# Kernel optimization log

Measured on AMD Instinct MI355X. Metric: run time of the kernel, lower is better.

Reference implementation:

```python
import jax, jax.numpy as jnp
import numpy as np

EMBED_DIM = 1024
NUM_HEADS = 16
HEAD_DIM = EMBED_DIM // NUM_HEADS


def setup_inputs() -> dict:
    key = jax.random.key(0)
    ks = jax.random.split(key, 7)
    B, S, E = 2, 2048, EMBED_DIM
    # xavier_uniform bound for square [E, E] weight
    bound = float(np.sqrt(6.0 / (E + E)))
    mkw = lambda k: jax.random.uniform(k, (E, E), jnp.float32, -bound, bound)
    return {
        "query": jax.random.normal(ks[0], (B, S, E), jnp.float32),
        "key": jax.random.normal(ks[1], (B, S, E), jnp.float32),
        "value": jax.random.normal(ks[2], (B, S, E), jnp.float32),
        "Wq": mkw(ks[3]),
        "Wk": mkw(ks[4]),
        "Wv": mkw(ks[5]),
        "Wo": mkw(ks[6]),
    }


def reference(query, key, value, Wq, Wk, Wv, Wo):
    # Chunked sigmoid attention: since sigmoid has no cross-key normalization
    # and all projections are bias-free linear maps, summing per-KV-chunk
    # partial outputs is mathematically identical to the full computation:
    #   out = (sigmoid(scale * Q K^T) @ V) @ Wo^T
    B, L, E = query.shape
    H, D = NUM_HEADS, HEAD_DIM
    scale = D ** -0.5
    q = (query @ Wq.T).reshape(B, L, H, D) * scale   # [B,L,H,D]
    k = (key @ Wk.T).reshape(B, -1, H, D)            # [B,S,H,D]
    v = (value @ Wv.T).reshape(B, -1, H, D)          # [B,S,H,D]
    scores = jax.nn.sigmoid(jnp.einsum('blhd,bshd->bhls', q, k))  # [B,H,L,S]
    o = jnp.einsum('bhls,bshd->blhd', scores, v).reshape(B, L, E)
    return o @ Wo.T
```

## Files before the change

kernel.cpp:

```cpp
#include <hip/hip_runtime.h>

typedef float f32x4 __attribute__((ext_vector_type(4)));
typedef float f32x16 __attribute__((ext_vector_type(16)));
typedef __bf16 bf16x4 __attribute__((ext_vector_type(4)));
typedef __bf16 bf16x8 __attribute__((ext_vector_type(8)));

constexpr int E = 1024;
constexpr int S = 2048;
constexpr int Bsz = 2;
constexpr int H = 16;
constexpr int Dh = 64;
constexpr int M = Bsz * S;
constexpr int E2 = 2048;

#define GLOAD_LDS16(g, l)                                                                 \
  __builtin_amdgcn_global_load_lds((const __attribute__((address_space(1))) void*)(g),    \
                                   (__attribute__((address_space(3))) void*)(l), 16, 0, 0)

__device__ __forceinline__ unsigned pk2(float a, float b) {
  union { __bf16 h[2]; unsigned u; } r;
  r.h[0] = (__bf16)a; r.h[1] = (__bf16)b;
  return r.u;
}

__global__ __launch_bounds__(256) void convert_bf16(
    const float* __restrict__ q, const float* __restrict__ k,
    const float* __restrict__ v, const float* __restrict__ wq,
    const float* __restrict__ wk, const float* __restrict__ wv,
    const float* __restrict__ wo, __bf16* __restrict__ aq,
    __bf16* __restrict__ ak, __bf16* __restrict__ av,
    __bf16* __restrict__ wqkv, __bf16* __restrict__ wob) {
  const int id = blockIdx.y;
  const float* src;
  __bf16* dst;
  int n;
  float scale = 1.0f;
  switch (id) {
    case 0: src = q;  dst = aq;             n = M * E; break;
    case 1: src = k;  dst = ak;             n = M * E; break;
    case 2: src = v;  dst = av;             n = M * E; break;
    case 3: src = wq; dst = wqkv;           n = E * E; scale = -0.18033688f; break;
    case 4: src = wk; dst = wqkv + E * E;   n = E * E; break;
    case 5: src = wv; dst = wqkv + 2 * E * E; n = E * E; break;
    default: src = wo; dst = wob;           n = E * E; break;
  }
  const int stride = gridDim.x * 256 * 8;
  for (int i = (blockIdx.x * 256 + threadIdx.x) * 8; i < n; i += stride) {
    f32x4 a = *reinterpret_cast<const f32x4*>(&src[i]);
    f32x4 b = *reinterpret_cast<const f32x4*>(&src[i + 4]);
    bf16x8 o;
    o[0] = (__bf16)(a[0] * scale); o[1] = (__bf16)(a[1] * scale);
    o[2] = (__bf16)(a[2] * scale); o[3] = (__bf16)(a[3] * scale);
    o[4] = (__bf16)(b[0] * scale); o[5] = (__bf16)(b[1] * scale);
    o[6] = (__bf16)(b[2] * scale); o[7] = (__bf16)(b[3] * scale);
    *reinterpret_cast<bf16x8*>(&dst[i]) = o;
  }
}

template <int TM, int MODE, int KS>
__global__ __launch_bounds__(256) void gemm_bf16nt(
    const __bf16* __restrict__ A0, const __bf16* __restrict__ A1,
    const __bf16* __restrict__ A2, const __bf16* __restrict__ Bw,
    void* __restrict__ C0, void* __restrict__ C1, void* __restrict__ C2) {
  static_assert(TM == 64, "vmcnt literal assumes TM=64 (6 chunks/wave)");
  constexpr int MI  = TM / 32;
  constexpr int NT  = KS / 64;
  constexpr int ACH = TM / 8;
  constexpr int NCH = ACH + 16;
  constexpr int NTN = (MODE == 0) ? 24 : 8;
  constexpr int NWG = NTN * (M / TM);
  constexpr int CPX = NWG / 8;

  __shared__ char smem[2][NCH * 1024];

  const int t    = threadIdx.x;
  const int lane = t & 63;
  const int wid  = t >> 6;
  const int wr   = (wid >> 1) * (TM / 2);
  const int wc   = (wid & 1) * 64;
  const int r16  = lane & 15;

  const int bid = blockIdx.x;
  const int fid = (bid & 7) * CPX + (bid >> 3);
  const int mt  = fid / NTN;
  const int nt  = fid % NTN;
  const int tm  = mt * TM;
  const int tn  = nt * 128;
  const int which = tn >> 10;

  const __bf16* Ab = (MODE == 0) ? (which == 0 ? A0 : which == 1 ? A1 : A2) : A0;

  auto stage = [&](int kt, int buf) {
    const int k0  = kt * 64;
    const int k0b = k0 & 1023;
    char* dst = smem[buf];
#pragma unroll
    for (int c = wid; c < NCH; c += 4) {
      const bool isA = c < ACH;
      const int cc   = isA ? c : c - ACH;
      const int L    = cc * 1024 + lane * 16;
      const int row  = L >> 7;
      const int sw   = ((L >> 4) & 7) ^ (row & 7);
      const __bf16* src = isA ? &Ab[(size_t)(tm + row) * KS + k0 + sw * 8]
                              : &Bw[(size_t)(tn + row) * 1024 + k0b + sw * 8];
      GLOAD_LDS16(src, dst + c * 1024);
    }
  };

  stage(0, 0);
  stage(1, 1);

  f32x4 acc[MI][4] = {};

  for (int kt = 0; kt < NT; ++kt) {
    const int buf = kt & 1;
    if (kt + 1 < NT) {
      asm volatile("s_waitcnt vmcnt(6)" ::: "memory");
    } else {
      asm volatile("s_waitcnt vmcnt(0)" ::: "memory");
    }
    __builtin_amdgcn_s_barrier();
    __builtin_amdgcn_sched_barrier(0);

    const __bf16* As = (const __bf16*)smem[buf];
    const __bf16* Bs = (const __bf16*)(smem[buf] + ACH * 1024);

#pragma unroll
    for (int kc = 0; kc < 2; ++kc) {
      bf16x8 af[MI], bfv[4];
#pragma unroll
      for (int mi = 0; mi < MI; ++mi) {
        int row = wr + mi * 16 + r16;
        int g   = (kc * 4 + (lane >> 4)) ^ (row & 7);
        af[mi] = *reinterpret_cast<const bf16x8*>(&As[row * 64 + g * 8]);
      }
#pragma unroll
      for (int ni = 0; ni < 4; ++ni) {
        int row = wc + ni * 16 + r16;
        int g   = (kc * 4 + (lane >> 4)) ^ (row & 7);
        bfv[ni] = *reinterpret_cast<const bf16x8*>(&Bs[row * 64 + g * 8]);
      }
      __builtin_amdgcn_s_setprio(1);
#pragma unroll
      for (int mi = 0; mi < MI; ++mi)
#pragma unroll
        for (int ni = 0; ni < 4; ++ni)
          acc[mi][ni] = __builtin_amdgcn_mfma_f32_16x16x32_bf16(af[mi], bfv[ni],
                                                                acc[mi][ni], 0, 0, 0);
      __builtin_amdgcn_s_setprio(0);
    }

    __builtin_amdgcn_sched_barrier(0);
    __builtin_amdgcn_s_barrier();
    if (kt + 2 < NT) stage(kt + 2, buf);
  }

#pragma unroll
  for (int mi = 0; mi < MI; ++mi) {
#pragma unroll
    for (int ni = 0; ni < 4; ++ni) {
#pragma unroll
      for (int j = 0; j < 4; ++j) {
        float v = acc[mi][ni][j];
        int m = tm + wr + mi * 16 + ((lane >> 4) << 2) + j;
        int n = tn + wc + ni * 16 + r16;
        if constexpr (MODE == 0) {
          int nl = n & 1023;
          int b = m >> 11, s = m & 2047, h = nl >> 6, d = nl & 63;
          __bf16* Cout = which == 0 ? (__bf16*)C0 : which == 1 ? (__bf16*)C1
                                                              : (__bf16*)C2;
          if (which < 2) {
            Cout[((size_t)(b * H + h) * S + s) * Dh + d] = (__bf16)v;
          } else {
            int ssw = (s & ~12) | ((s & 4) << 1) | ((s & 8) >> 1);
            Cout[((size_t)(b * H + h) * Dh + d) * S + ssw] = (__bf16)v;
          }
        } else {
          ((float*)C0)[(size_t)m * E + n] = v;
        }
      }
    }
  }
}

__global__ __launch_bounds__(128, 4) void attn_sigmoid(const __bf16* __restrict__ Q,
                                                       const __bf16* __restrict__ K,
                                                       const __bf16* __restrict__ Vt,
                                                       __bf16* __restrict__ O) {
  __shared__ char smem[16384];

  const int t    = threadIdx.x;
  const int lane = t & 63;
  const int qgrp = t >> 6;
  const int l31  = lane & 31;
  const int hh   = lane >> 5;
  const int qt   = blockIdx.x >> 1;
  const int ss   = blockIdx.x & 1;
  const int q0   = qt * 64;
  const int h    = blockIdx.y;
  const int b    = blockIdx.z;

  const __bf16* Qh = Q + (size_t)(b * H + h) * S * Dh;
  const __bf16* Kh = K + (size_t)(b * H + h) * S * Dh;
  const __bf16* Vh = Vt + (size_t)(b * H + h) * Dh * S;

  const __bf16* kSrc = Kh + (size_t)(ss * 1024 + (lane >> 3)) * Dh +
                       (((lane & 7) ^ (lane >> 3)) * 8);
  const __bf16* vSrc = Vh + (size_t)(lane >> 2) * S + ss * 1024 +
                       (((lane & 3) ^ ((lane >> 3) & 3)) * 8);

  auto stage = [&](int it, int buf) {
    char* dst = smem + buf * 8192;
    if (qgrp == 0) {
#pragma unroll
      for (int j = 0; j < 4; ++j)
        GLOAD_LDS16(kSrc + it * 2048 + j * 512, dst + j * 1024);
    } else {
#pragma unroll
      for (int j = 0; j < 4; ++j)
        GLOAD_LDS16(vSrc + it * 32 + (size_t)j * 16 * S, dst + 4096 + j * 1024);
    }
  };

  bf16x8 Qf[4];
#pragma unroll
  for (int kc = 0; kc < 4; ++kc)
    Qf[kc] = *reinterpret_cast<const bf16x8*>(
        &Qh[(size_t)(q0 + qgrp * 32 + l31) * Dh + kc * 16 + hh * 8]);

  stage(0, 0);
  stage(1, 1);

  f32x16 ot0 = {}, ot1 = {};

#pragma unroll 2
  for (int it = 0; it < 32; ++it) {
    const int buf = it & 1;
    if (it + 1 < 32) {
      asm volatile("s_waitcnt vmcnt(4)" ::: "memory");
    } else {
      asm volatile("s_waitcnt vmcnt(0)" ::: "memory");
    }
    __builtin_amdgcn_s_barrier();
    __builtin_amdgcn_sched_barrier(0);

    const __bf16* Kb = (const __bf16*)(smem + buf * 8192);
    const __bf16* Vb = (const __bf16*)(smem + buf * 8192 + 4096);

    bf16x8 kf[4], vf[4];
#pragma unroll
    for (int kc = 0; kc < 4; ++kc) {
      int x = (2 * kc + hh) ^ (l31 & 7);
      kf[kc] = *reinterpret_cast<const bf16x8*>(&Kb[l31 * 64 + x * 8]);
    }
#pragma unroll
    for (int kc2 = 0; kc2 < 2; ++kc2)
#pragma unroll
      for (int dblk = 0; dblk < 2; ++dblk) {
        int row = dblk * 32 + l31;
        int x   = (2 * kc2 + hh) ^ ((l31 >> 1) & 3);
        vf[kc2 * 2 + dblk] = *reinterpret_cast<const bf16x8*>(&Vb[row * 32 + x * 8]);
      }

    f32x16 sacc = {};
    __builtin_amdgcn_s_setprio(1);
#pragma unroll
    for (int kc = 0; kc < 4; ++kc)
      sacc = __builtin_amdgcn_mfma_f32_32x32x16_bf16(kf[kc], Qf[kc], sacc, 0, 0, 0);
    __builtin_amdgcn_s_setprio(0);

    bf16x8 F[2];
    {
      union { unsigned u[4]; bf16x8 v; } fu[2];
#pragma unroll
      for (int kc2 = 0; kc2 < 2; ++kc2) {
#pragma unroll
        for (int jj = 0; jj < 4; ++jj) {
          float ya = sacc[kc2 * 8 + 2 * jj];
          float yb = sacc[kc2 * 8 + 2 * jj + 1];
          float pa = __builtin_amdgcn_rcpf(1.0f + __builtin_amdgcn_exp2f(ya));
          float pb = __builtin_amdgcn_rcpf(1.0f + __builtin_amdgcn_exp2f(yb));
          fu[kc2].u[jj] = pk2(pa, pb);
        }
        F[kc2] = fu[kc2].v;
      }
    }

    __builtin_amdgcn_s_setprio(1);
    ot0 = __builtin_amdgcn_mfma_f32_32x32x16_bf16(vf[0], F[0], ot0, 0, 0, 0);
    ot1 = __builtin_amdgcn_mfma_f32_32x32x16_bf16(vf[1], F[0], ot1, 0, 0, 0);
    ot0 = __builtin_amdgcn_mfma_f32_32x32x16_bf16(vf[2], F[1], ot0, 0, 0, 0);
    ot1 = __builtin_amdgcn_mfma_f32_32x32x16_bf16(vf[3], F[1], ot1, 0, 0, 0);
    __builtin_amdgcn_s_setprio(0);

    __builtin_amdgcn_sched_barrier(0);
    __builtin_amdgcn_s_barrier();
    if (it + 2 < 32) stage(it + 2, buf);
  }

  __bf16* Os = (__bf16*)smem;
  {
    int row = qgrp * 32 + l31;
#pragma unroll
    for (int dblk = 0; dblk < 2; ++dblk)
#pragma unroll
      for (int rp = 0; rp < 4; ++rp) {
        int r  = rp * 4;
        int g  = dblk * 4 + rp;
        int by = row * 128 + ((g ^ (row & 7)) * 16) + hh * 8;
        float a0 = dblk ? ot1[r]     : ot0[r];
        float a1 = dblk ? ot1[r + 1] : ot0[r + 1];
        float a2 = dblk ? ot1[r + 2] : ot0[r + 2];
        float a3 = dblk ? ot1[r + 3] : ot0[r + 3];
        unsigned long long val =
            (unsigned long long)pk2(a0, a1) | ((unsigned long long)pk2(a2, a3) << 32);
        *reinterpret_cast<unsigned long long*>((char*)Os + by) = val;
      }
  }
  __syncthreads();
#pragma unroll
  for (int i = 0; i < 4; ++i) {
    int c   = i * 128 + t;
    int row = c >> 3;
    int ch  = c & 7;
    bf16x8 v = *reinterpret_cast<const bf16x8*>(
        (char*)Os + row * 128 + ((ch ^ (row & 7)) * 16));
    *reinterpret_cast<bf16x8*>(
        &O[((size_t)(b * S) + q0 + row) * E2 + ss * 1024 + h * Dh + ch * 8]) = v;
  }
}

extern "C" void kernel_launch(void* const* d_in, const int* in_sizes, int n_in,
                              void* d_out, int out_size, void* d_ws, size_t ws_size,
                              hipStream_t stream) {
  const float* query = (const float*)d_in[0];
  const float* key_  = (const float*)d_in[1];
  const float* value = (const float*)d_in[2];
  const float* Wq    = (const float*)d_in[3];
  const float* Wk    = (const float*)d_in[4];
  const float* Wv    = (const float*)d_in[5];
  const float* Wo    = (const float*)d_in[6];

  char* ws = (char*)d_ws;
  __bf16* aq   = (__bf16*)(ws);
  __bf16* ak   = (__bf16*)(ws + ((size_t)8 << 20));
  __bf16* av   = (__bf16*)(ws + ((size_t)16 << 20));
  __bf16* wqkv = (__bf16*)(ws + ((size_t)24 << 20));
  __bf16* wob  = (__bf16*)(ws + ((size_t)30 << 20));
  __bf16* pq   = (__bf16*)(ws + ((size_t)32 << 20));
  __bf16* pk   = (__bf16*)(ws + ((size_t)40 << 20));
  __bf16* pvt  = (__bf16*)(ws + ((size_t)48 << 20));
  __bf16* ob   = (__bf16*)(ws);

  convert_bf16<<<dim3(512, 7), 256, 0, stream>>>(query, key_, value, Wq, Wk, Wv,
                                                 Wo, aq, ak, av, wqkv, wob);

  gemm_bf16nt<64, 0, 1024><<<1536, 256, 0, stream>>>(
      aq, ak, av, wqkv, pq, pk, pvt);

  attn_sigmoid<<<dim3(S / 32, H, Bsz), 128, 0, stream>>>(pq, pk, pvt, ob);

  gemm_bf16nt<64, 2, 2048><<<512, 256, 0, stream>>>(
      ob, nullptr, nullptr, wob, (float*)d_out, nullptr, nullptr);
}
```

Before: 144.8 us.

## Load attention K/V tiles directly to registers and shrink GEMM K-step

The attention kernel drops its LDS staging and barriers for K and V. Each wave now loads its K/V fragments straight from global memory into registers, double-buffered in software. To keep those loads contiguous, the QKV GEMM epilogue writes V^T in a blocked layout of 32-column tiles. The GEMM K-tile is halved to 32 with a k-group-major LDS layout in place of the XOR swizzle, and occupancy hints are set. This removes LDS traffic and synchronisation but duplicates global loads across the two waves, raises register pressure, and may add LDS bank conflicts in the GEMM.

```diff
diff --git a/kernel.cpp b/kernel.cpp
--- a/kernel.cpp
+++ b/kernel.cpp
@@ -57,28 +57,27 @@
   }
 }
 
-template <int TM, int MODE, int KS>
-__global__ __launch_bounds__(256) void gemm_bf16nt(
+template <int MODE, int KS>
+__global__ __launch_bounds__(256, 6) void gemm_bf16nt(
     const __bf16* __restrict__ A0, const __bf16* __restrict__ A1,
     const __bf16* __restrict__ A2, const __bf16* __restrict__ Bw,
     void* __restrict__ C0, void* __restrict__ C1, void* __restrict__ C2) {
-  static_assert(TM == 64, "vmcnt literal assumes TM=64 (6 chunks/wave)");
-  constexpr int MI  = TM / 32;
-  constexpr int NT  = KS / 64;
-  constexpr int ACH = TM / 8;
-  constexpr int NCH = ACH + 16;
+  constexpr int TM  = 64;
+  constexpr int MI  = 2;
+  constexpr int NT  = KS / 32;
   constexpr int NTN = (MODE == 0) ? 24 : 8;
   constexpr int NWG = NTN * (M / TM);
   constexpr int CPX = NWG / 8;
 
-  __shared__ char smem[2][NCH * 1024];
+  __shared__ char smem[2][12288];
 
   const int t    = threadIdx.x;
   const int lane = t & 63;
   const int wid  = t >> 6;
-  const int wr   = (wid >> 1) * (TM / 2);
+  const int wr   = (wid >> 1) * 32;
   const int wc   = (wid & 1) * 64;
   const int r16  = lane & 15;
+  const int g4   = lane >> 4;
 
   const int bid = blockIdx.x;
   const int fid = (bid & 7) * CPX + (bid >> 3);
@@ -91,18 +90,19 @@
   const __bf16* Ab = (MODE == 0) ? (which == 0 ? A0 : which == 1 ? A1 : A2) : A0;
 
   auto stage = [&](int kt, int buf) {
-    const int k0  = kt * 64;
+    const int k0  = kt * 32;
     const int k0b = k0 & 1023;
     char* dst = smem[buf];
 #pragma unroll
-    for (int c = wid; c < NCH; c += 4) {
-      const bool isA = c < ACH;
-      const int cc   = isA ? c : c - ACH;
-      const int L    = cc * 1024 + lane * 16;
-      const int row  = L >> 7;
-      const int sw   = ((L >> 4) & 7) ^ (row & 7);
-      const __bf16* src = isA ? &Ab[(size_t)(tm + row) * KS + k0 + sw * 8]
-                              : &Bw[(size_t)(tn + row) * 1024 + k0b + sw * 8];
+    for (int j = 0; j < 3; ++j) {
+      const int c = wid + 4 * j;
+      const __bf16* src;
+      if (c < 4) {
+        src = &Ab[(size_t)(tm + lane) * KS + k0 + c * 8];
+      } else {
+        const int cb = c - 4;
+        src = &Bw[(size_t)(tn + (cb & 1) * 64 + lane) * 1024 + k0b + (cb >> 1) * 8];
+      }
       GLOAD_LDS16(src, dst + c * 1024);
     }
   };
@@ -115,40 +115,34 @@
   for (int kt = 0; kt < NT; ++kt) {
     const int buf = kt & 1;
     if (kt + 1 < NT) {
-      asm volatile("s_waitcnt vmcnt(6)" ::: "memory");
+      asm volatile("s_waitcnt vmcnt(3)" ::: "memory");
     } else {
       asm volatile("s_waitcnt vmcnt(0)" ::: "memory");
     }
     __builtin_amdgcn_s_barrier();
     __builtin_amdgcn_sched_barrier(0);
 
-    const __bf16* As = (const __bf16*)smem[buf];
-    const __bf16* Bs = (const __bf16*)(smem[buf] + ACH * 1024);
-
-#pragma unroll
-    for (int kc = 0; kc < 2; ++kc) {
-      bf16x8 af[MI], bfv[4];
-#pragma unroll
-      for (int mi = 0; mi < MI; ++mi) {
-        int row = wr + mi * 16 + r16;
-        int g   = (kc * 4 + (lane >> 4)) ^ (row & 7);
-        af[mi] = *reinterpret_cast<const bf16x8*>(&As[row * 64 + g * 8]);
-      }
-#pragma unroll
-      for (int ni = 0; ni < 4; ++ni) {
-        int row = wc + ni * 16 + r16;
-        int g   = (kc * 4 + (lane >> 4)) ^ (row & 7);
-        bfv[ni] = *reinterpret_cast<const bf16x8*>(&Bs[row * 64 + g * 8]);
-      }
-      __builtin_amdgcn_s_setprio(1);
-#pragma unroll
-      for (int mi = 0; mi < MI; ++mi)
-#pragma unroll
-        for (int ni = 0; ni < 4; ++ni)
-          acc[mi][ni] = __builtin_amdgcn_mfma_f32_16x16x32_bf16(af[mi], bfv[ni],
-                                                                acc[mi][ni], 0, 0, 0);
-      __builtin_amdgcn_s_setprio(0);
-    }
+    const char* As = smem[buf];
+    const char* Bs = smem[buf] + 4096;
+
+    bf16x8 af[MI], bfv[4];
+#pragma unroll
+    for (int mi = 0; mi < MI; ++mi)
+      af[mi] = *reinterpret_cast<const bf16x8*>(
+          As + g4 * 1024 + (wr + mi * 16 + r16) * 16);
+#pragma unroll
+    for (int ni = 0; ni < 4; ++ni)
+      bfv[ni] = *reinterpret_cast<const bf16x8*>(
+          Bs + g4 * 2048 + (wc + ni * 16 + r16) * 16);
+
+    __builtin_amdgcn_s_setprio(1);
+#pragma unroll
+    for (int mi = 0; mi < MI; ++mi)
+#pragma unroll
+      for (int ni = 0; ni < 4; ++ni)
+        acc[mi][ni] = __builtin_amdgcn_mfma_f32_16x16x32_bf16(af[mi], bfv[ni],
+                                                              acc[mi][ni], 0, 0, 0);
+    __builtin_amdgcn_s_setprio(0);
 
     __builtin_amdgcn_sched_barrier(0);
     __builtin_amdgcn_s_barrier();
@@ -173,7 +167,8 @@
             Cout[((size_t)(b * H + h) * S + s) * Dh + d] = (__bf16)v;
           } else {
             int ssw = (s & ~12) | ((s & 4) << 1) | ((s & 8) >> 1);
-            Cout[((size_t)(b * H + h) * Dh + d) * S + ssw] = (__bf16)v;
+            Cout[(((size_t)(b * H + h) * 64 + (s >> 5)) * 64 + d) * 32 + (ssw & 31)] =
+                (__bf16)v;
           }
         } else {
           ((float*)C0)[(size_t)m * E + n] = v;
@@ -183,11 +178,11 @@
   }
 }
 
-__global__ __launch_bounds__(128, 4) void attn_sigmoid(const __bf16* __restrict__ Q,
+__global__ __launch_bounds__(128, 3) void attn_sigmoid(const __bf16* __restrict__ Q,
                                                        const __bf16* __restrict__ K,
                                                        const __bf16* __restrict__ Vt,
                                                        __bf16* __restrict__ O) {
-  __shared__ char smem[16384];
+  __shared__ char smem[8192];
 
   const int t    = threadIdx.x;
   const int lane = t & 63;
@@ -201,26 +196,10 @@
   const int b    = blockIdx.z;
 
   const __bf16* Qh = Q + (size_t)(b * H + h) * S * Dh;
-  const __bf16* Kh = K + (size_t)(b * H + h) * S * Dh;
-  const __bf16* Vh = Vt + (size_t)(b * H + h) * Dh * S;
-
-  const __bf16* kSrc = Kh + (size_t)(ss * 1024 + (lane >> 3)) * Dh +
-                       (((lane & 7) ^ (lane >> 3)) * 8);
-  const __bf16* vSrc = Vh + (size_t)(lane >> 2) * S + ss * 1024 +
-                       (((lane & 3) ^ ((lane >> 3) & 3)) * 8);
-
-  auto stage = [&](int it, int buf) {
-    char* dst = smem + buf * 8192;
-    if (qgrp == 0) {
-#pragma unroll
-      for (int j = 0; j < 4; ++j)
-        GLOAD_LDS16(kSrc + it * 2048 + j * 512, dst + j * 1024);
-    } else {
-#pragma unroll
-      for (int j = 0; j < 4; ++j)
-        GLOAD_LDS16(vSrc + it * 32 + (size_t)j * 16 * S, dst + 4096 + j * 1024);
-    }
-  };
+  const __bf16* kp = K + (size_t)(b * H + h) * S * Dh +
+                     (size_t)(ss * 1024 + l31) * Dh + hh * 8;
+  const __bf16* vp = Vt + ((size_t)(b * H + h) * 64 + ss * 32) * 2048 +
+                     l31 * 32 + hh * 8;
 
   bf16x8 Qf[4];
 #pragma unroll
@@ -228,40 +207,21 @@
     Qf[kc] = *reinterpret_cast<const bf16x8*>(
         &Qh[(size_t)(q0 + qgrp * 32 + l31) * Dh + kc * 16 + hh * 8]);
 
-  stage(0, 0);
-  stage(1, 1);
+  auto loadT = [&](int it, bf16x8 (&kf)[4], bf16x8 (&vf)[4]) {
+    const __bf16* kq = kp + (size_t)it * 32 * Dh;
+    const __bf16* vq = vp + (size_t)it * 2048;
+#pragma unroll
+    for (int kc = 0; kc < 4; ++kc)
+      kf[kc] = *reinterpret_cast<const bf16x8*>(kq + kc * 16);
+    vf[0] = *reinterpret_cast<const bf16x8*>(vq);
+    vf[1] = *reinterpret_cast<const bf16x8*>(vq + 1024);
+    vf[2] = *reinterpret_cast<const bf16x8*>(vq + 16);
+    vf[3] = *reinterpret_cast<const bf16x8*>(vq + 1040);
+  };
 
   f32x16 ot0 = {}, ot1 = {};
 
-#pragma unroll 2
-  for (int it = 0; it < 32; ++it) {
-    const int buf = it & 1;
-    if (it + 1 < 32) {
-      asm volatile("s_waitcnt vmcnt(4)" ::: "memory");
-    } else {
-      asm volatile("s_waitcnt vmcnt(0)" ::: "memory");
-    }
-    __builtin_amdgcn_s_barrier();
-    __builtin_amdgcn_sched_barrier(0);
-
-    const __bf16* Kb = (const __bf16*)(smem + buf * 8192);
-    const __bf16* Vb = (const __bf16*)(smem + buf * 8192 + 4096);
-
-    bf16x8 kf[4], vf[4];
-#pragma unroll
-    for (int kc = 0; kc < 4; ++kc) {
-      int x = (2 * kc + hh) ^ (l31 & 7);
-      kf[kc] = *reinterpret_cast<const bf16x8*>(&Kb[l31 * 64 + x * 8]);
-    }
-#pragma unroll
-    for (int kc2 = 0; kc2 < 2; ++kc2)
-#pragma unroll
-      for (int dblk = 0; dblk < 2; ++dblk) {
-        int row = dblk * 32 + l31;
-        int x   = (2 * kc2 + hh) ^ ((l31 >> 1) & 3);
-        vf[kc2 * 2 + dblk] = *reinterpret_cast<const bf16x8*>(&Vb[row * 32 + x * 8]);
-      }
-
+  auto compute = [&](bf16x8 (&kf)[4], bf16x8 (&vf)[4]) {
     f32x16 sacc = {};
     __builtin_amdgcn_s_setprio(1);
 #pragma unroll
@@ -270,20 +230,18 @@
     __builtin_amdgcn_s_setprio(0);
 
     bf16x8 F[2];
-    {
-      union { unsigned u[4]; bf16x8 v; } fu[2];
-#pragma unroll
-      for (int kc2 = 0; kc2 < 2; ++kc2) {
-#pragma unroll
-        for (int jj = 0; jj < 4; ++jj) {
-          float ya = sacc[kc2 * 8 + 2 * jj];
-          float yb = sacc[kc2 * 8 + 2 * jj + 1];
-          float pa = __builtin_amdgcn_rcpf(1.0f + __builtin_amdgcn_exp2f(ya));
-          float pb = __builtin_amdgcn_rcpf(1.0f + __builtin_amdgcn_exp2f(yb));
-          fu[kc2].u[jj] = pk2(pa, pb);
-        }
-        F[kc2] = fu[kc2].v;
+    union { unsigned u[4]; bf16x8 v; } fu[2];
+#pragma unroll
+    for (int kc2 = 0; kc2 < 2; ++kc2) {
+#pragma unroll
+      for (int jj = 0; jj < 4; ++jj) {
+        float ya = sacc[kc2 * 8 + 2 * jj];
+        float yb = sacc[kc2 * 8 + 2 * jj + 1];
+        float pa = __builtin_amdgcn_rcpf(1.0f + __builtin_amdgcn_exp2f(ya));
+        float pb = __builtin_amdgcn_rcpf(1.0f + __builtin_amdgcn_exp2f(yb));
+        fu[kc2].u[jj] = pk2(pa, pb);
       }
+      F[kc2] = fu[kc2].v;
     }
 
     __builtin_amdgcn_s_setprio(1);
@@ -292,10 +250,17 @@
     ot0 = __builtin_amdgcn_mfma_f32_32x32x16_bf16(vf[2], F[1], ot0, 0, 0, 0);
     ot1 = __builtin_amdgcn_mfma_f32_32x32x16_bf16(vf[3], F[1], ot1, 0, 0, 0);
     __builtin_amdgcn_s_setprio(0);
-
-    __builtin_amdgcn_sched_barrier(0);
-    __builtin_amdgcn_s_barrier();
-    if (it + 2 < 32) stage(it + 2, buf);
+  };
+
+  bf16x8 kA[4], vA[4], kB[4], vB[4];
+  loadT(0, kA, vA);
+
+#pragma unroll 2
+  for (int it = 0; it < 32; it += 2) {
+    if (it + 1 < 32) loadT(it + 1, kB, vB);
+    compute(kA, vA);
+    if (it + 2 < 32) loadT(it + 2, kA, vA);
+    compute(kB, vB);
   }
 
   __bf16* Os = (__bf16*)smem;
@@ -355,11 +320,11 @@
   convert_bf16<<<dim3(512, 7), 256, 0, stream>>>(query, key_, value, Wq, Wk, Wv,
                                                  Wo, aq, ak, av, wqkv, wob);
 
-  gemm_bf16nt<64, 0, 1024><<<1536, 256, 0, stream>>>(
+  gemm_bf16nt<0, 1024><<<1536, 256, 0, stream>>>(
       aq, ak, av, wqkv, pq, pk, pvt);
 
   attn_sigmoid<<<dim3(S / 32, H, Bsz), 128, 0, stream>>>(pq, pk, pvt, ob);
 
-  gemm_bf16nt<64, 2, 2048><<<512, 256, 0, stream>>>(
+  gemm_bf16nt<2, 2048><<<512, 256, 0, stream>>>(
       ob, nullptr, nullptr, wob, (float*)d_out, nullptr, nullptr);
 }
```

Result: slower. 266.4 us (+84.0%).

## Use single-wave attention blocks to drop per-iteration barriers and reuse K/V fragments

Applied to the files above, without the earlier changes.

The attention kernel moves from two waves per block, each owning 32 query rows, to one wave handling all 64 rows with two accumulator sets. Because only one wave touches shared memory, the per-iteration s_barrier calls go away, and the next stage's K/V loads are issued right after the fragments are read into registers, so the prefetch starts earlier. Each K/V fragment now feeds twice as many MFMAs, at the cost of more registers per wave (launch bounds now 64 threads, min 2 blocks per CU) and fewer waves available to hide latency.

```diff
diff --git a/kernel.cpp b/kernel.cpp
--- a/kernel.cpp
+++ b/kernel.cpp
@@ -183,15 +183,14 @@
   }
 }
 
-__global__ __launch_bounds__(128, 4) void attn_sigmoid(const __bf16* __restrict__ Q,
-                                                       const __bf16* __restrict__ K,
-                                                       const __bf16* __restrict__ Vt,
-                                                       __bf16* __restrict__ O) {
+__global__ __launch_bounds__(64, 2) void attn_sigmoid(const __bf16* __restrict__ Q,
+                                                      const __bf16* __restrict__ K,
+                                                      const __bf16* __restrict__ Vt,
+                                                      __bf16* __restrict__ O) {
   __shared__ char smem[16384];
 
   const int t    = threadIdx.x;
   const int lane = t & 63;
-  const int qgrp = t >> 6;
   const int l31  = lane & 31;
   const int hh   = lane >> 5;
   const int qt   = blockIdx.x >> 1;
@@ -211,37 +210,35 @@
 
   auto stage = [&](int it, int buf) {
     char* dst = smem + buf * 8192;
-    if (qgrp == 0) {
-#pragma unroll
-      for (int j = 0; j < 4; ++j)
-        GLOAD_LDS16(kSrc + it * 2048 + j * 512, dst + j * 1024);
-    } else {
-#pragma unroll
-      for (int j = 0; j < 4; ++j)
-        GLOAD_LDS16(vSrc + it * 32 + (size_t)j * 16 * S, dst + 4096 + j * 1024);
-    }
+#pragma unroll
+    for (int j = 0; j < 4; ++j)
+      GLOAD_LDS16(kSrc + it * 2048 + j * 512, dst + j * 1024);
+#pragma unroll
+    for (int j = 0; j < 4; ++j)
+      GLOAD_LDS16(vSrc + it * 32 + (size_t)j * 16 * S, dst + 4096 + j * 1024);
   };
 
-  bf16x8 Qf[4];
-#pragma unroll
-  for (int kc = 0; kc < 4; ++kc)
-    Qf[kc] = *reinterpret_cast<const bf16x8*>(
-        &Qh[(size_t)(q0 + qgrp * 32 + l31) * Dh + kc * 16 + hh * 8]);
+  bf16x8 Qf[2][4];
+#pragma unroll
+  for (int g = 0; g < 2; ++g)
+#pragma unroll
+    for (int kc = 0; kc < 4; ++kc)
+      Qf[g][kc] = *reinterpret_cast<const bf16x8*>(
+          &Qh[(size_t)(q0 + g * 32 + l31) * Dh + kc * 16 + hh * 8]);
 
   stage(0, 0);
   stage(1, 1);
 
-  f32x16 ot0 = {}, ot1 = {};
+  f32x16 ot[2][2] = {};
 
 #pragma unroll 2
   for (int it = 0; it < 32; ++it) {
     const int buf = it & 1;
     if (it + 1 < 32) {
-      asm volatile("s_waitcnt vmcnt(4)" ::: "memory");
+      asm volatile("s_waitcnt vmcnt(8)" ::: "memory");
     } else {
       asm volatile("s_waitcnt vmcnt(0)" ::: "memory");
     }
-    __builtin_amdgcn_s_barrier();
     __builtin_amdgcn_sched_barrier(0);
 
     const __bf16* Kb = (const __bf16*)(smem + buf * 8192);
@@ -261,57 +258,68 @@
         int x   = (2 * kc2 + hh) ^ ((l31 >> 1) & 3);
         vf[kc2 * 2 + dblk] = *reinterpret_cast<const bf16x8*>(&Vb[row * 32 + x * 8]);
       }
-
-    f32x16 sacc = {};
+    asm volatile("s_waitcnt lgkmcnt(0)" ::: "memory");
+    __builtin_amdgcn_sched_barrier(0);
+
+    if (it + 2 < 32) stage(it + 2, buf);
+
+    f32x16 s0 = {}, s1 = {};
     __builtin_amdgcn_s_setprio(1);
 #pragma unroll
-    for (int kc = 0; kc < 4; ++kc)
-      sacc = __builtin_amdgcn_mfma_f32_32x32x16_bf16(kf[kc], Qf[kc], sacc, 0, 0, 0);
+    for (int kc = 0; kc < 4; ++kc) {
+      s0 = __builtin_amdgcn_mfma_f32_32x32x16_bf16(kf[kc], Qf[0][kc], s0, 0, 0, 0);
+      s1 = __builtin_amdgcn_mfma_f32_32x32x16_bf16(kf[kc], Qf[1][kc], s1, 0, 0, 0);
+    }
     __builtin_amdgcn_s_setprio(0);
 
-    bf16x8 F[2];
-    {
+    bf16x8 F[2][2];
+#pragma unroll
+    for (int g = 0; g < 2; ++g) {
       union { unsigned u[4]; bf16x8 v; } fu[2];
 #pragma unroll
       for (int kc2 = 0; kc2 < 2; ++kc2) {
 #pragma unroll
         for (int jj = 0; jj < 4; ++jj) {
-          float ya = sacc[kc2 * 8 + 2 * jj];
-          float yb = sacc[kc2 * 8 + 2 * jj + 1];
+          float ya = g ? s1[kc2 * 8 + 2 * jj] : s0[kc2 * 8 + 2 * jj];
+          float yb = g ? s1[kc2 * 8 + 2 * jj + 1] : s0[kc2 * 8 + 2 * jj + 1];
           float pa = __builtin_amdgcn_rcpf(1.0f + __builtin_amdgcn_exp2f(ya));
           float pb = __builtin_amdgcn_rcpf(1.0f + __builtin_amdgcn_exp2f(yb));
           fu[kc2].u[jj] = pk2(pa, pb);
         }
-        F[kc2] = fu[kc2].v;
+        F[g][kc2] = fu[kc2].v;
       }
     }
 
     __builtin_amdgcn_s_setprio(1);
-    ot0 = __builtin_amdgcn_mfma_f32_32x32x16_bf16(vf[0], F[0], ot0, 0, 0, 0);
-    ot1 = __builtin_amdgcn_mfma_f32_32x32x16_bf16(vf[1], F[0], ot1, 0, 0, 0);
-    ot0 = __builtin_amdgcn_mfma_f32_32x32x16_bf16(vf[2], F[1], ot0, 0, 0, 0);
-    ot1 = __builtin_amdgcn_mfma_f32_32x32x16_bf16(vf[3], F[1], ot1, 0, 0, 0);
+#pragma unroll
+    for (int kc2 = 0; kc2 < 2; ++kc2) {
+#pragma unroll
+      for (int dblk = 0; dblk < 2; ++dblk) {
+        ot[0][dblk] = __builtin_amdgcn_mfma_f32_32x32x16_bf16(
+            vf[kc2 * 2 + dblk], F[0][kc2], ot[0][dblk], 0, 0, 0);
+        ot[1][dblk] = __builtin_amdgcn_mfma_f32_32x32x16_bf16(
+            vf[kc2 * 2 + dblk], F[1][kc2], ot[1][dblk], 0, 0, 0);
+      }
+    }
     __builtin_amdgcn_s_setprio(0);
-
-    __builtin_amdgcn_sched_barrier(0);
-    __builtin_amdgcn_s_barrier();
-    if (it + 2 < 32) stage(it + 2, buf);
-  }
-
+  }
+
+  __syncthreads();
   __bf16* Os = (__bf16*)smem;
-  {
-    int row = qgrp * 32 + l31;
+#pragma unroll
+  for (int g = 0; g < 2; ++g) {
+    int row = g * 32 + l31;
 #pragma unroll
     for (int dblk = 0; dblk < 2; ++dblk)
 #pragma unroll
       for (int rp = 0; rp < 4; ++rp) {
         int r  = rp * 4;
-        int g  = dblk * 4 + rp;
-        int by = row * 128 + ((g ^ (row & 7)) * 16) + hh * 8;
-        float a0 = dblk ? ot1[r]     : ot0[r];
-        float a1 = dblk ? ot1[r + 1] : ot0[r + 1];
-        float a2 = dblk ? ot1[r + 2] : ot0[r + 2];
-        float a3 = dblk ? ot1[r + 3] : ot0[r + 3];
+        int gg = dblk * 4 + rp;
+        int by = row * 128 + ((gg ^ (row & 7)) * 16) + hh * 8;
+        float a0 = ot[g][dblk][r];
+        float a1 = ot[g][dblk][r + 1];
+        float a2 = ot[g][dblk][r + 2];
+        float a3 = ot[g][dblk][r + 3];
         unsigned long long val =
             (unsigned long long)pk2(a0, a1) | ((unsigned long long)pk2(a2, a3) << 32);
         *reinterpret_cast<unsigned long long*>((char*)Os + by) = val;
@@ -319,8 +327,8 @@
   }
   __syncthreads();
 #pragma unroll
-  for (int i = 0; i < 4; ++i) {
-    int c   = i * 128 + t;
+  for (int i = 0; i < 8; ++i) {
+    int c   = i * 64 + t;
     int row = c >> 3;
     int ch  = c & 7;
     bf16x8 v = *reinterpret_cast<const bf16x8*>(
@@ -358,7 +366,7 @@
   gemm_bf16nt<64, 0, 1024><<<1536, 256, 0, stream>>>(
       aq, ak, av, wqkv, pq, pk, pvt);
 
-  attn_sigmoid<<<dim3(S / 32, H, Bsz), 128, 0, stream>>>(pq, pk, pvt, ob);
+  attn_sigmoid<<<dim3(S / 32, H, Bsz), 64, 0, stream>>>(pq, pk, pvt, ob);
 
   gemm_bf16nt<64, 2, 2048><<<512, 256, 0, stream>>>(
       ob, nullptr, nullptr, wob, (float*)d_out, nullptr, nullptr);
```

After: 142.7 us. Within noise of the previous version (-1.4%).

## Use single-wave attention blocks with single-buffered LDS and no barriers

Applied to the files above, without the earlier changes.

The sigmoid attention kernel shrinks from two waves covering 64 queries to one wave covering 32 queries, which doubles the grid. Because each block is now a single wave, the s_barrier calls go away. LDS is single-buffered: the wave waits for the current K/V tile, pulls it into registers, then issues the next tile's global-to-LDS load so it overlaps with the MFMA and sigmoid work. The cost is that K/V tiles are loaded from global memory twice as often per query, and there is less prefetch depth than with double buffering.

```diff
diff --git a/kernel.cpp b/kernel.cpp
--- a/kernel.cpp
+++ b/kernel.cpp
@@ -183,20 +183,19 @@
   }
 }
 
-__global__ __launch_bounds__(128, 4) void attn_sigmoid(const __bf16* __restrict__ Q,
-                                                       const __bf16* __restrict__ K,
-                                                       const __bf16* __restrict__ Vt,
-                                                       __bf16* __restrict__ O) {
-  __shared__ char smem[16384];
+__global__ __launch_bounds__(64, 4) void attn_sigmoid(const __bf16* __restrict__ Q,
+                                                      const __bf16* __restrict__ K,
+                                                      const __bf16* __restrict__ Vt,
+                                                      __bf16* __restrict__ O) {
+  __shared__ char smem[8192];
 
   const int t    = threadIdx.x;
   const int lane = t & 63;
-  const int qgrp = t >> 6;
   const int l31  = lane & 31;
   const int hh   = lane >> 5;
   const int qt   = blockIdx.x >> 1;
   const int ss   = blockIdx.x & 1;
-  const int q0   = qt * 64;
+  const int q0   = qt * 32;
   const int h    = blockIdx.y;
   const int b    = blockIdx.z;
 
@@ -209,43 +208,32 @@
   const __bf16* vSrc = Vh + (size_t)(lane >> 2) * S + ss * 1024 +
                        (((lane & 3) ^ ((lane >> 3) & 3)) * 8);
 
-  auto stage = [&](int it, int buf) {
-    char* dst = smem + buf * 8192;
-    if (qgrp == 0) {
-#pragma unroll
-      for (int j = 0; j < 4; ++j)
-        GLOAD_LDS16(kSrc + it * 2048 + j * 512, dst + j * 1024);
-    } else {
-#pragma unroll
-      for (int j = 0; j < 4; ++j)
-        GLOAD_LDS16(vSrc + it * 32 + (size_t)j * 16 * S, dst + 4096 + j * 1024);
-    }
+  auto stage = [&](int it) {
+#pragma unroll
+    for (int j = 0; j < 4; ++j)
+      GLOAD_LDS16(kSrc + it * 2048 + j * 512, smem + j * 1024);
+#pragma unroll
+    for (int j = 0; j < 4; ++j)
+      GLOAD_LDS16(vSrc + it * 32 + (size_t)j * 16 * S, smem + 4096 + j * 1024);
   };
 
   bf16x8 Qf[4];
 #pragma unroll
   for (int kc = 0; kc < 4; ++kc)
     Qf[kc] = *reinterpret_cast<const bf16x8*>(
-        &Qh[(size_t)(q0 + qgrp * 32 + l31) * Dh + kc * 16 + hh * 8]);
-
-  stage(0, 0);
-  stage(1, 1);
+        &Qh[(size_t)(q0 + l31) * Dh + kc * 16 + hh * 8]);
+
+  stage(0);
 
   f32x16 ot0 = {}, ot1 = {};
 
 #pragma unroll 2
   for (int it = 0; it < 32; ++it) {
-    const int buf = it & 1;
-    if (it + 1 < 32) {
-      asm volatile("s_waitcnt vmcnt(4)" ::: "memory");
-    } else {
-      asm volatile("s_waitcnt vmcnt(0)" ::: "memory");
-    }
-    __builtin_amdgcn_s_barrier();
+    asm volatile("s_waitcnt vmcnt(0)" ::: "memory");
     __builtin_amdgcn_sched_barrier(0);
 
-    const __bf16* Kb = (const __bf16*)(smem + buf * 8192);
-    const __bf16* Vb = (const __bf16*)(smem + buf * 8192 + 4096);
+    const __bf16* Kb = (const __bf16*)smem;
+    const __bf16* Vb = (const __bf16*)(smem + 4096);
 
     bf16x8 kf[4], vf[4];
 #pragma unroll
@@ -261,6 +249,10 @@
         int x   = (2 * kc2 + hh) ^ ((l31 >> 1) & 3);
         vf[kc2 * 2 + dblk] = *reinterpret_cast<const bf16x8*>(&Vb[row * 32 + x * 8]);
       }
+    asm volatile("s_waitcnt lgkmcnt(0)" ::: "memory");
+    __builtin_amdgcn_sched_barrier(0);
+
+    if (it + 1 < 32) stage(it + 1);
 
     f32x16 sacc = {};
     __builtin_amdgcn_s_setprio(1);
@@ -292,15 +284,12 @@
     ot0 = __builtin_amdgcn_mfma_f32_32x32x16_bf16(vf[2], F[1], ot0, 0, 0, 0);
     ot1 = __builtin_amdgcn_mfma_f32_32x32x16_bf16(vf[3], F[1], ot1, 0, 0, 0);
     __builtin_amdgcn_s_setprio(0);
-
-    __builtin_amdgcn_sched_barrier(0);
-    __builtin_amdgcn_s_barrier();
-    if (it + 2 < 32) stage(it + 2, buf);
-  }
-
+  }
+
+  __syncthreads();
   __bf16* Os = (__bf16*)smem;
   {
-    int row = qgrp * 32 + l31;
+    int row = l31;
 #pragma unroll
     for (int dblk = 0; dblk < 2; ++dblk)
 #pragma unroll
@@ -320,7 +309,7 @@
   __syncthreads();
 #pragma unroll
   for (int i = 0; i < 4; ++i) {
-    int c   = i * 128 + t;
+    int c   = i * 64 + t;
     int row = c >> 3;
     int ch  = c & 7;
     bf16x8 v = *reinterpret_cast<const bf16x8*>(
@@ -358,7 +347,7 @@
   gemm_bf16nt<64, 0, 1024><<<1536, 256, 0, stream>>>(
       aq, ak, av, wqkv, pq, pk, pvt);
 
-  attn_sigmoid<<<dim3(S / 32, H, Bsz), 128, 0, stream>>>(pq, pk, pvt, ob);
+  attn_sigmoid<<<dim3(S / 16, H, Bsz), 64, 0, stream>>>(pq, pk, pvt, ob);
 
   gemm_bf16nt<64, 2, 2048><<<512, 256, 0, stream>>>(
       ob, nullptr, nullptr, wob, (float*)d_out, nullptr, nullptr);
```

New measurement: 154.0 us. +6.4%, slower.
